# Kernel tuning notes

Hardware: AMD Instinct MI355X
Metric: run time of the kernel (lower is better)

## Reference

```python
import jax, jax.numpy as jnp
import numpy as np

HEADS = 16
EMBED = 1024
HEAD_DIM = EMBED // HEADS


def setup_inputs() -> dict:
    k = jax.random.key(0)
    ks = jax.random.split(k, 8)
    N, L = 8, 1024
    s = 1.0 / np.sqrt(HEAD_DIM)
    return {
        "key": jax.random.normal(ks[0], (N, L, EMBED), jnp.float32),
        "query": jax.random.normal(ks[1], (N, L, EMBED), jnp.float32),
        "value": jax.random.normal(ks[2], (N, L, EMBED), jnp.float32),
        "mask": jnp.ones((N, 1, 1, L), jnp.int32),
        "Wq": jax.random.normal(ks[3], (HEAD_DIM, HEAD_DIM), jnp.float32) * s,
        "Wk": jax.random.normal(ks[4], (HEAD_DIM, HEAD_DIM), jnp.float32) * s,
        "Wv": jax.random.normal(ks[5], (HEAD_DIM, HEAD_DIM), jnp.float32) * s,
        "Wo": jax.random.normal(ks[6], (EMBED, EMBED), jnp.float32) * (1.0 / np.sqrt(EMBED)),
    }


def reference(key, query, value, mask, Wq, Wk, Wv, Wo):
    # NOTE: original torch code calls weights.masked_fill(...) without assignment,
    # which is a no-op, so `mask` is faithfully ignored here.
    N, Lq, E = query.shape
    Lk = key.shape[1]
    H, D = HEADS, E // HEADS
    q = query.reshape(N, Lq, H, D)
    k = key.reshape(N, Lk, H, D)
    v = value.reshape(N, Lk, H, D)
    # per-head linear with weight shared across heads: x @ W^T (torch Linear)
    q = jnp.einsum('nqhd,ed->nqhe', q, Wq)
    k = jnp.einsum('nkhd,ed->nkhe', k, Wk)
    v = jnp.einsum('nkhd,ed->nkhe', v, Wv)
    weights = jnp.einsum('nqhd,nkhd->nhqk', q, k)
    attn = jax.nn.softmax(weights / jnp.sqrt(jnp.asarray(E, weights.dtype)), axis=-1)
    out = jnp.einsum('nhqk,nkhd->nqhd', attn, v).reshape(N, Lq, E)
    return out @ Wo.T
```

## Files before the change

### kernel.cpp

```cpp
#include <hip/hip_runtime.h>
#include <hip/hip_bf16.h>

#define HEADS 16
#define HDIM  64
#define EMB   1024
#define NB    8
#define SEQ   1024

typedef __bf16 bf16_t;
typedef __bf16 bf16x8 __attribute__((ext_vector_type(8)));
typedef __bf16 bf16x4 __attribute__((ext_vector_type(4)));
typedef float  floatx4 __attribute__((ext_vector_type(4)));
typedef float  f32x16  __attribute__((ext_vector_type(16)));

union PkU { unsigned u; __bf16 h[2]; };
union W4U { unsigned u[4]; bf16x8 v; };

__device__ __forceinline__ bf16x8 load8bf(const bf16_t* p) { return *(const bf16x8*)p; }
__device__ __forceinline__ bf16x4 cvt4(float4 a) {
    bf16x4 r; r[0]=(bf16_t)a.x; r[1]=(bf16_t)a.y; r[2]=(bf16_t)a.z; r[3]=(bf16_t)a.w;
    return r;
}
__device__ __forceinline__ bf16x8 cvt8(float4 a, float4 b) {
    bf16x8 r;
    r[0]=(bf16_t)a.x; r[1]=(bf16_t)a.y; r[2]=(bf16_t)a.z; r[3]=(bf16_t)a.w;
    r[4]=(bf16_t)b.x; r[5]=(bf16_t)b.y; r[6]=(bf16_t)b.z; r[7]=(bf16_t)b.w;
    return r;
}

__global__ __launch_bounds__(256) void proj_kernel(
    const float* __restrict__ q_in, const float* __restrict__ k_in,
    const float* __restrict__ v_in,
    const float* __restrict__ Wq, const float* __restrict__ Wk,
    const float* __restrict__ Wv,
    bf16_t* __restrict__ qp, bf16_t* __restrict__ kp, bf16_t* __restrict__ vt)
{
    __shared__ __align__(16) bf16_t wl[64][72];
    __shared__ __align__(16) bf16_t lo[64][72];

    const int wave = threadIdx.x >> 6;
    const int lane = threadIdx.x & 63;
    const int m  = lane & 15;
    const int q4 = lane >> 4;
    const int op = blockIdx.y;

    const float* x = (op == 0) ? q_in : (op == 1) ? k_in : v_in;
    const float* W = (op == 0) ? Wq   : (op == 1) ? Wk   : Wv;

    {
        const int t  = threadIdx.x;
        const int f  = t >> 2;
        const int kg = (t & 3) * 16;
        #pragma unroll
        for (int j = 0; j < 4; ++j) {
            float4 v = *(const float4*)(W + f * 64 + kg + j * 4);
            *(bf16x4*)&wl[f][kg + j * 4] = cvt4(v);
        }
    }
    __syncthreads();

    if (op == 2) {
        const int nh = blockIdx.x >> 4;
        const int l0 = (blockIdx.x & 15) * 64;
        const int n  = nh >> 4;
        const int h  = nh & 15;

        const int la = l0 + wave * 16 + m;
        const float* xr = x + (size_t)(n * 16384 + la * 16 + h) * 64;
        float4 f0 = *(const float4*)(xr + q4 * 8);
        float4 f1 = *(const float4*)(xr + q4 * 8 + 4);
        float4 f2 = *(const float4*)(xr + 32 + q4 * 8);
        float4 f3 = *(const float4*)(xr + 32 + q4 * 8 + 4);
        bf16x8 a0 = cvt8(f0, f1);
        bf16x8 a1 = cvt8(f2, f3);

        floatx4 acc[4];
        #pragma unroll
        for (int sub = 0; sub < 4; ++sub) {
            bf16x8 b0 = load8bf(&wl[sub * 16 + m][q4 * 8]);
            bf16x8 b1 = load8bf(&wl[sub * 16 + m][32 + q4 * 8]);
            floatx4 z = {0.f, 0.f, 0.f, 0.f};
            z = __builtin_amdgcn_mfma_f32_16x16x32_bf16(a0, b0, z, 0, 0, 0);
            z = __builtin_amdgcn_mfma_f32_16x16x32_bf16(a1, b1, z, 0, 0, 0);
            acc[sub] = z;
        }

        #pragma unroll
        for (int sub = 0; sub < 4; ++sub) {
            #pragma unroll
            for (int r = 0; r < 4; r += 2) {
                PkU u; u.h[0] = (bf16_t)acc[sub][r]; u.h[1] = (bf16_t)acc[sub][r + 1];
                *(unsigned*)&lo[sub * 16 + m][wave * 16 + q4 * 4 + r] = u.u;
            }
        }
        __syncthreads();

        const int e  = threadIdx.x >> 2;
        const int lc = (threadIdx.x & 3) * 16;
        bf16_t* dst = vt + ((size_t)nh * 64 + e) * 1024 + l0 + lc;
        *(bf16x8*)dst       = *(const bf16x8*)&lo[e][lc];
        *(bf16x8*)(dst + 8) = *(const bf16x8*)&lo[e][lc + 8];
    } else {
        const int row0 = blockIdx.x * 64 + wave * 16;

        const float* xr = x + (size_t)(row0 + m) * 64;
        float4 f0 = *(const float4*)(xr + q4 * 8);
        float4 f1 = *(const float4*)(xr + q4 * 8 + 4);
        float4 f2 = *(const float4*)(xr + 32 + q4 * 8);
        float4 f3 = *(const float4*)(xr + 32 + q4 * 8 + 4);
        bf16x8 a0 = cvt8(f0, f1);
        bf16x8 a1 = cvt8(f2, f3);

        floatx4 acc[4];
        #pragma unroll
        for (int sub = 0; sub < 4; ++sub) {
            bf16x8 b0 = load8bf(&wl[sub * 16 + m][q4 * 8]);
            bf16x8 b1 = load8bf(&wl[sub * 16 + m][32 + q4 * 8]);
            floatx4 z = {0.f, 0.f, 0.f, 0.f};
            z = __builtin_amdgcn_mfma_f32_16x16x32_bf16(a0, b0, z, 0, 0, 0);
            z = __builtin_amdgcn_mfma_f32_16x16x32_bf16(a1, b1, z, 0, 0, 0);
            acc[sub] = z;
        }

        #pragma unroll
        for (int sub = 0; sub < 4; ++sub) {
            #pragma unroll
            for (int r = 0; r < 4; ++r) {
                lo[wave * 16 + q4 * 4 + r][sub * 16 + m] = (bf16_t)acc[sub][r];
            }
        }
        __syncthreads();

        const int gl = threadIdx.x >> 2;
        const int ec = (threadIdx.x & 3) * 16;
        const int g  = blockIdx.x * 64 + gl;
        const int n  = g >> 14;
        const int l  = (g >> 4) & 1023;
        const int h  = g & 15;
        const int nh = n * 16 + h;
        bf16_t* dst = ((op == 0) ? qp : kp) + ((size_t)nh * 1024 + l) * 64 + ec;
        *(bf16x8*)dst       = *(const bf16x8*)&lo[gl][ec];
        *(bf16x8*)(dst + 8) = *(const bf16x8*)&lo[gl][ec + 8];
    }
}

__global__ __launch_bounds__(256) void attn_kernel(
    bf16_t* __restrict__ qp, const bf16_t* __restrict__ kp,
    const bf16_t* __restrict__ vt)
{
    __shared__ __align__(16) bf16_t kl[2][64][64];
    __shared__ __align__(16) bf16_t vl[2][64][64];

    const int lane = threadIdx.x & 63;
    const int wave = threadIdx.x >> 6;
    const int q32  = lane & 31;
    const int hi   = lane >> 5;

    const int nh   = blockIdx.x & 127;
    const int qblk = blockIdx.x >> 7;

    bf16_t* Q = qp + (size_t)nh * 65536;
    const bf16_t* K = kp + (size_t)nh * 65536;
    const bf16_t* V = vt + (size_t)nh * 65536;

    const int qb = qblk * 128 + wave * 32;

    const int srow  = lane >> 3;
    const int sslot = lane & 7;
    const int ch    = sslot ^ srow;

    auto stage = [&](int b, int kb) {
        #pragma unroll
        for (int i = 0; i < 2; ++i) {
            const int rbase = wave * 16 + i * 8;
            const int row   = rbase + srow;
            __builtin_amdgcn_global_load_lds(
                (const __attribute__((address_space(1))) unsigned int*)(K + (size_t)(kb + row) * 64 + ch * 8),
                (__attribute__((address_space(3))) unsigned int*)(&kl[b][rbase][0]),
                16, 0, 0);
            __builtin_amdgcn_global_load_lds(
                (const __attribute__((address_space(1))) unsigned int*)(V + (size_t)row * 1024 + kb + ch * 8),
                (__attribute__((address_space(3))) unsigned int*)(&vl[b][rbase][0]),
                16, 0, 0);
        }
    };

    stage(0, 0);

    bf16x8 bq[4];
    #pragma unroll
    for (int sl = 0; sl < 4; ++sl)
        bq[sl] = load8bf(Q + (size_t)(qb + q32) * 64 + sl * 16 + hi * 8);

    f32x16 o0 = {0.f,0.f,0.f,0.f,0.f,0.f,0.f,0.f,0.f,0.f,0.f,0.f,0.f,0.f,0.f,0.f};
    f32x16 o1 = o0;
    float lsum = 0.f;
    const float CE = 1.4426950408889634f * 0.03125f;

    int cur = 0;
    __syncthreads();

    for (int kt = 0; kt < 16; ++kt) {
        if (kt < 15) stage(cur ^ 1, (kt + 1) * 64);

        #pragma unroll
        for (int kb32 = 0; kb32 < 2; ++kb32) {
            const int krow = kb32 * 32 + q32;
            f32x16 s = {0.f,0.f,0.f,0.f,0.f,0.f,0.f,0.f,0.f,0.f,0.f,0.f,0.f,0.f,0.f,0.f};
            __builtin_amdgcn_s_setprio(1);
            #pragma unroll
            for (int sl = 0; sl < 4; ++sl) {
                const int ck = ((sl * 2 + hi) ^ (krow & 7)) * 8;
                bf16x8 ka = load8bf(&kl[cur][krow][ck]);
                s = __builtin_amdgcn_mfma_f32_32x32x16_bf16(ka, bq[sl], s, 0, 0, 0);
            }
            __builtin_amdgcn_s_setprio(0);

            unsigned w[8];
            #pragma unroll
            for (int t = 0; t < 8; ++t) {
                float p0 = exp2f(s[2 * t]     * CE);
                float p1 = exp2f(s[2 * t + 1] * CE);
                lsum += p0 + p1;
                PkU u; u.h[0] = (bf16_t)p0; u.h[1] = (bf16_t)p1;
                w[t] = u.u;
            }

            bf16x8 va[4];
            #pragma unroll
            for (int db = 0; db < 2; ++db) {
                const int d = db * 32 + q32;
                #pragma unroll
                for (int c = 0; c < 2; ++c) {
                    const int cv = ((kb32 * 4 + c * 2 + hi) ^ (d & 7)) * 8;
                    va[db * 2 + c] = load8bf(&vl[cur][d][cv]);
                }
            }

            const unsigned e0 = (unsigned)__shfl_xor((int)(hi ? w[0] : w[2]), 32, 64);
            const unsigned e1 = (unsigned)__shfl_xor((int)(hi ? w[1] : w[3]), 32, 64);
            const unsigned e2 = (unsigned)__shfl_xor((int)(hi ? w[4] : w[6]), 32, 64);
            const unsigned e3 = (unsigned)__shfl_xor((int)(hi ? w[5] : w[7]), 32, 64);

            W4U b0v, b1v;
            b0v.u[0] = hi ? e0 : w[0];
            b0v.u[1] = hi ? e1 : w[1];
            b0v.u[2] = hi ? w[2] : e0;
            b0v.u[3] = hi ? w[3] : e1;
            b1v.u[0] = hi ? e2 : w[4];
            b1v.u[1] = hi ? e3 : w[5];
            b1v.u[2] = hi ? w[6] : e2;
            b1v.u[3] = hi ? w[7] : e3;

            __builtin_amdgcn_s_setprio(1);
            o0 = __builtin_amdgcn_mfma_f32_32x32x16_bf16(va[0], b0v.v, o0, 0, 0, 0);
            o0 = __builtin_amdgcn_mfma_f32_32x32x16_bf16(va[1], b1v.v, o0, 0, 0, 0);
            o1 = __builtin_amdgcn_mfma_f32_32x32x16_bf16(va[2], b0v.v, o1, 0, 0, 0);
            o1 = __builtin_amdgcn_mfma_f32_32x32x16_bf16(va[3], b1v.v, o1, 0, 0, 0);
            __builtin_amdgcn_s_setprio(0);
        }

        __syncthreads();
        cur ^= 1;
    }

    lsum += __shfl_xor(lsum, 32, 64);
    const float inv = 1.0f / lsum;

    #pragma unroll
    for (int g = 0; g < 4; ++g) {
        bf16x4 w0v, w1v;
        #pragma unroll
        for (int r = 0; r < 4; ++r) {
            w0v[r] = (bf16_t)(o0[g * 4 + r] * inv);
            w1v[r] = (bf16_t)(o1[g * 4 + r] * inv);
        }
        *(bf16x4*)(Q + (size_t)(qb + q32) * 64 +      g * 8 + hi * 4) = w0v;
        *(bf16x4*)(Q + (size_t)(qb + q32) * 64 + 32 + g * 8 + hi * 4) = w1v;
    }
}

__global__ __launch_bounds__(256) void wocvt_kernel(
    const float* __restrict__ Wo, bf16_t* __restrict__ wo_bf)
{
    const int i = (blockIdx.x * 256 + threadIdx.x) * 8;
    float4 f0 = *(const float4*)(Wo + i);
    float4 f1 = *(const float4*)(Wo + i + 4);
    *(bf16x8*)(wo_bf + i) = cvt8(f0, f1);
}

__global__ __launch_bounds__(256) void outproj_kernel(
    const bf16_t* __restrict__ aoq, const bf16_t* __restrict__ wo_bf,
    float* __restrict__ out)
{
    __shared__ __align__(16) bf16_t wl[64][72];

    const int wave = threadIdx.x >> 6;
    const int lane = threadIdx.x & 63;
    const int m  = lane & 15;
    const int q4 = lane >> 4;

    const int by = blockIdx.x & 15;
    const int bx = blockIdx.x >> 4;

    const int row0 = bx * 128 + wave * 32;
    const int col0 = by * 64;

    const int ts_f  = threadIdx.x >> 2;
    const int ts_kg = (threadIdx.x & 3) * 16;

    floatx4 acc[2][4];
    #pragma unroll
    for (int rs = 0; rs < 2; ++rs)
        #pragma unroll
        for (int cs = 0; cs < 4; ++cs) acc[rs][cs] = (floatx4){0.f, 0.f, 0.f, 0.f};

    for (int h = 0; h < 16; ++h) {
        const int kc = h * 64;
        __syncthreads();
        *(bf16x8*)&wl[ts_f][ts_kg] =
            load8bf(wo_bf + (size_t)(col0 + ts_f) * 1024 + kc + ts_kg);
        *(bf16x8*)&wl[ts_f][ts_kg + 8] =
            load8bf(wo_bf + (size_t)(col0 + ts_f) * 1024 + kc + ts_kg + 8);
        __syncthreads();

        bf16x8 a[2][2];
        #pragma unroll
        for (int rs = 0; rs < 2; ++rs) {
            const int g = row0 + rs * 16 + m;
            const int n = g >> 10;
            const int q = g & 1023;
            const bf16_t* arow = aoq + ((size_t)(n * 16 + h) * 1024 + q) * 64;
            a[rs][0] = load8bf(arow + q4 * 8);
            a[rs][1] = load8bf(arow + 32 + q4 * 8);
        }

        #pragma unroll
        for (int cs = 0; cs < 4; ++cs) {
            bf16x8 b0 = load8bf(&wl[cs * 16 + m][q4 * 8]);
            bf16x8 b1 = load8bf(&wl[cs * 16 + m][32 + q4 * 8]);
            #pragma unroll
            for (int rs = 0; rs < 2; ++rs) {
                acc[rs][cs] = __builtin_amdgcn_mfma_f32_16x16x32_bf16(a[rs][0], b0, acc[rs][cs], 0, 0, 0);
                acc[rs][cs] = __builtin_amdgcn_mfma_f32_16x16x32_bf16(a[rs][1], b1, acc[rs][cs], 0, 0, 0);
            }
        }
    }

    #pragma unroll
    for (int rs = 0; rs < 2; ++rs) {
        #pragma unroll
        for (int r = 0; r < 4; ++r) {
            const int g = row0 + rs * 16 + q4 * 4 + r;
            #pragma unroll
            for (int cs = 0; cs < 4; ++cs)
                out[(size_t)g * 1024 + col0 + cs * 16 + m] = acc[rs][cs][r];
        }
    }
}

extern "C" void kernel_launch(void* const* d_in, const int* in_sizes, int n_in,
                              void* d_out, int out_size, void* d_ws, size_t ws_size,
                              hipStream_t stream) {
    const float* key   = (const float*)d_in[0];
    const float* query = (const float*)d_in[1];
    const float* value = (const float*)d_in[2];
    const float* Wq = (const float*)d_in[4];
    const float* Wk = (const float*)d_in[5];
    const float* Wv = (const float*)d_in[6];
    const float* Wo = (const float*)d_in[7];

    const size_t TENS = (size_t)NB * SEQ * EMB;
    bf16_t* qp = (bf16_t*)d_ws;
    bf16_t* vt = qp + TENS;
    bf16_t* kp = (bf16_t*)d_out;

    hipLaunchKernelGGL(proj_kernel, dim3(2048, 3), dim3(256), 0, stream,
                       query, key, value, Wq, Wk, Wv, qp, kp, vt);
    hipLaunchKernelGGL(attn_kernel, dim3(1024), dim3(256), 0, stream, qp, kp, vt);
    hipLaunchKernelGGL(wocvt_kernel, dim3(512), dim3(256), 0, stream, Wo, vt);
    hipLaunchKernelGGL(outproj_kernel, dim3(1024), dim3(256), 0, stream,
                       qp, vt, (float*)d_out);
}
```

Baseline: 261.1 us.

## Fold softmax scale into Q projection, use permlane32 swap and MFMA row sums

Pre-multiplies the Q projection output by the log2e/sqrt(E) softmax scale, so the attention loop computes exp2 directly on the scores. The ds_swizzle-style shuffles plus selects are replaced by permlane32_swap, and the per-lane scalar softmax denominator accumulation is replaced by extra MFMAs against a ones vector. This removes VALU multiplies and adds, plus cross-lane shuffles, at the cost of two additional MFMAs per 32-key block. It also rounds the scaled Q to bf16 and sums the bf16-rounded probabilities, which slightly changes numerics.

```diff
diff --git a/kernel.cpp b/kernel.cpp
--- a/kernel.cpp
+++ b/kernel.cpp
@@ -12,6 +12,7 @@
 typedef __bf16 bf16x4 __attribute__((ext_vector_type(4)));
 typedef float  floatx4 __attribute__((ext_vector_type(4)));
 typedef float  f32x16  __attribute__((ext_vector_type(16)));
+typedef unsigned uint2v __attribute__((ext_vector_type(2)));
 
 union PkU { unsigned u; __bf16 h[2]; };
 union W4U { unsigned u[4]; bf16x8 v; };
@@ -101,6 +102,7 @@
         *(bf16x8*)dst       = *(const bf16x8*)&lo[e][lc];
         *(bf16x8*)(dst + 8) = *(const bf16x8*)&lo[e][lc + 8];
     } else {
+        const float qscale = (op == 0) ? (1.4426950408889634f * 0.03125f) : 1.0f;
         const int row0 = blockIdx.x * 64 + wave * 16;
 
         const float* xr = x + (size_t)(row0 + m) * 64;
@@ -126,7 +128,7 @@
         for (int sub = 0; sub < 4; ++sub) {
             #pragma unroll
             for (int r = 0; r < 4; ++r) {
-                lo[wave * 16 + q4 * 4 + r][sub * 16 + m] = (bf16_t)acc[sub][r];
+                lo[wave * 16 + q4 * 4 + r][sub * 16 + m] = (bf16_t)(acc[sub][r] * qscale);
             }
         }
         __syncthreads();
@@ -192,10 +194,13 @@
     for (int sl = 0; sl < 4; ++sl)
         bq[sl] = load8bf(Q + (size_t)(qb + q32) * 64 + sl * 16 + hi * 8);
 
+    bf16x8 ones;
+    #pragma unroll
+    for (int j = 0; j < 8; ++j) ones[j] = (bf16_t)1.0f;
+
     f32x16 o0 = {0.f,0.f,0.f,0.f,0.f,0.f,0.f,0.f,0.f,0.f,0.f,0.f,0.f,0.f,0.f,0.f};
     f32x16 o1 = o0;
-    float lsum = 0.f;
-    const float CE = 1.4426950408889634f * 0.03125f;
+    f32x16 osum = o0;
 
     int cur = 0;
     __syncthreads();
@@ -219,9 +224,8 @@
             unsigned w[8];
             #pragma unroll
             for (int t = 0; t < 8; ++t) {
-                float p0 = exp2f(s[2 * t]     * CE);
-                float p1 = exp2f(s[2 * t + 1] * CE);
-                lsum += p0 + p1;
+                float p0 = exp2f(s[2 * t]);
+                float p1 = exp2f(s[2 * t + 1]);
                 PkU u; u.h[0] = (bf16_t)p0; u.h[1] = (bf16_t)p1;
                 w[t] = u.u;
             }
@@ -237,26 +241,23 @@
                 }
             }
 
-            const unsigned e0 = (unsigned)__shfl_xor((int)(hi ? w[0] : w[2]), 32, 64);
-            const unsigned e1 = (unsigned)__shfl_xor((int)(hi ? w[1] : w[3]), 32, 64);
-            const unsigned e2 = (unsigned)__shfl_xor((int)(hi ? w[4] : w[6]), 32, 64);
-            const unsigned e3 = (unsigned)__shfl_xor((int)(hi ? w[5] : w[7]), 32, 64);
-
             W4U b0v, b1v;
-            b0v.u[0] = hi ? e0 : w[0];
-            b0v.u[1] = hi ? e1 : w[1];
-            b0v.u[2] = hi ? w[2] : e0;
-            b0v.u[3] = hi ? w[3] : e1;
-            b1v.u[0] = hi ? e2 : w[4];
-            b1v.u[1] = hi ? e3 : w[5];
-            b1v.u[2] = hi ? w[6] : e2;
-            b1v.u[3] = hi ? w[7] : e3;
+            uint2v r02 = __builtin_amdgcn_permlane32_swap(w[0], w[2], false, false);
+            b0v.u[0] = r02[0]; b0v.u[2] = r02[1];
+            uint2v r13 = __builtin_amdgcn_permlane32_swap(w[1], w[3], false, false);
+            b0v.u[1] = r13[0]; b0v.u[3] = r13[1];
+            uint2v r46 = __builtin_amdgcn_permlane32_swap(w[4], w[6], false, false);
+            b1v.u[0] = r46[0]; b1v.u[2] = r46[1];
+            uint2v r57 = __builtin_amdgcn_permlane32_swap(w[5], w[7], false, false);
+            b1v.u[1] = r57[0]; b1v.u[3] = r57[1];
 
             __builtin_amdgcn_s_setprio(1);
             o0 = __builtin_amdgcn_mfma_f32_32x32x16_bf16(va[0], b0v.v, o0, 0, 0, 0);
             o0 = __builtin_amdgcn_mfma_f32_32x32x16_bf16(va[1], b1v.v, o0, 0, 0, 0);
             o1 = __builtin_amdgcn_mfma_f32_32x32x16_bf16(va[2], b0v.v, o1, 0, 0, 0);
             o1 = __builtin_amdgcn_mfma_f32_32x32x16_bf16(va[3], b1v.v, o1, 0, 0, 0);
+            osum = __builtin_amdgcn_mfma_f32_32x32x16_bf16(ones, b0v.v, osum, 0, 0, 0);
+            osum = __builtin_amdgcn_mfma_f32_32x32x16_bf16(ones, b1v.v, osum, 0, 0, 0);
             __builtin_amdgcn_s_setprio(0);
         }
 
@@ -264,8 +265,7 @@
         cur ^= 1;
     }
 
-    lsum += __shfl_xor(lsum, 32, 64);
-    const float inv = 1.0f / lsum;
+    const float inv = 1.0f / osum[0];
 
     #pragma unroll
     for (int g = 0; g < 4; ++g) {
```

Measured after the change: 257.2 us. Within noise of the previous version (-1.5%).
